# Optimization experiments

Measured on AMD Instinct MI355X. Metric: run time of the kernel, lower is better.

The kernel has to match this reference:

```python
import jax, jax.numpy as jnp
import numpy as np

K = 2048  # num_embeddings
D = 64    # embedding_dim


def setup_inputs() -> dict:
    key = jax.random.key(0)
    k1, k2 = jax.random.split(key)
    inputs = jax.random.normal(k1, (64, 32, 32, D), dtype=jnp.float32)
    # tf.random_uniform_initializer default: U[0, 1)
    embeddings = jax.random.uniform(k2, (K, D), dtype=jnp.float32)
    return {"inputs": inputs, "embeddings": embeddings}


def reference(inputs, embeddings):
    input_shape = inputs.shape
    flat_inputs = inputs.reshape(-1, D)  # [N, D]
    distances = (
        jnp.sum(flat_inputs ** 2, axis=1, keepdims=True)
        - 2.0 * jnp.matmul(flat_inputs, embeddings.T)
        + jnp.sum(embeddings ** 2, axis=1)
    )
    encoding_indices = jnp.argmin(distances, axis=1)  # [N]
    quantized = embeddings[encoding_indices].reshape(input_shape)
    # straight-through estimator
    quantized = inputs + jax.lax.stop_gradient(quantized - inputs)
    return quantized, encoding_indices, flat_inputs
```

## Files before the change

### kernel.cpp

```cpp
#include <hip/hip_runtime.h>
#include <cfloat>

#define N_TOTAL 65536
#define DIM     64
#define NEMB    2048

typedef __attribute__((ext_vector_type(8))) _Float16 half8;
typedef __attribute__((ext_vector_type(4))) float    floatx4;

__global__ void prep_kernel(const float* __restrict__ emb,
                            half8* __restrict__ ehp, float* __restrict__ en) {
    const int t = blockIdx.x * 256 + threadIdx.x;
    {
        const int l   = t & 63;
        const int ks  = (t >> 6) & 1;
        const int g   = t >> 7;
        const int col = g * 16 + (l & 15);
        const int kb  = ks * 32 + (l >> 4) * 8;
        const float* s = emb + col * DIM + kb;
        float4 v0 = *(const float4*)s, v1 = *(const float4*)(s + 4);
        half8 hv;
        hv[0] = (_Float16)v0.x; hv[1] = (_Float16)v0.y;
        hv[2] = (_Float16)v0.z; hv[3] = (_Float16)v0.w;
        hv[4] = (_Float16)v1.x; hv[5] = (_Float16)v1.y;
        hv[6] = (_Float16)v1.z; hv[7] = (_Float16)v1.w;
        ehp[t] = hv;
    }
    if (t < NEMB * 4) {
        const int row = t >> 2, seg = t & 3;
        const float* s = emb + row * DIM + seg * 16;
        float acc = 0.f;
#pragma unroll
        for (int i = 0; i < 4; ++i) {
            float4 v = ((const float4*)s)[i];
            acc = fmaf(v.x, v.x, acc); acc = fmaf(v.y, v.y, acc);
            acc = fmaf(v.z, v.z, acc); acc = fmaf(v.w, v.w, acc);
        }
        acc += __shfl_xor(acc, 1, 64);
        acc += __shfl_xor(acc, 2, 64);
        if (seg == 0) en[row] = acc;
    }
}

__global__ __launch_bounds__(256, 4) void vq_mfma_kernel(
        const float* __restrict__ x, const float* __restrict__ emb,
        const char* __restrict__ ehb, const float* __restrict__ eng,
        float* __restrict__ quant, float* __restrict__ idxf,
        float* __restrict__ flat) {

    __shared__ float EnS[NEMB];
    __shared__ uint4 Mrg[2][64];

    const int t    = threadIdx.x;
    const int wave = t >> 6, lane = t & 63;
    const int n = lane & 15, q = lane >> 4;
    const int h = wave & 1, p = wave >> 1;
    const int blk0 = blockIdx.x * 64;
    const int row0 = blk0 + p * 32;

    {
        const float4* s4 = (const float4*)(x + (size_t)blk0 * DIM);
        float4*       d4 = (float4*)(flat + (size_t)blk0 * DIM);
#pragma unroll
        for (int i = 0; i < 4; ++i) d4[i * 256 + t] = s4[i * 256 + t];
    }
    {
        const float4* s4 = (const float4*)eng;
        float4*       d4 = (float4*)EnS;
#pragma unroll
        for (int i = 0; i < 2; ++i) d4[i * 256 + t] = s4[i * 256 + t];
    }

    half8 ah[2][2], al[2][2];
#pragma unroll
    for (int tl = 0; tl < 2; ++tl)
#pragma unroll
        for (int ks = 0; ks < 2; ++ks) {
            const float* pp = x + (size_t)(row0 + tl * 16 + n) * DIM + ks * 32 + q * 8;
            float4 v0 = *(const float4*)pp, v1 = *(const float4*)(pp + 4);
            float xv[8] = {v0.x, v0.y, v0.z, v0.w, v1.x, v1.y, v1.z, v1.w};
#pragma unroll
            for (int j = 0; j < 8; ++j) {
                _Float16 hh = (_Float16)xv[j];
                ah[tl][ks][j] = hh;
                al[tl][ks][j] = (_Float16)(xv[j] - (float)hh);
            }
        }

    __syncthreads();

    unsigned best[8], sec[8];
#pragma unroll
    for (int r = 0; r < 8; ++r) { best[r] = 0u; sec[r] = 0u; }

    const char* ebase = ehb + (size_t)h * 131072 + (size_t)lane * 16;

    half8 bbuf[2][4];
    float enc[2][2];
#pragma unroll
    for (int i = 0; i < 4; ++i)
        bbuf[0][i] = *(const half8*)(ebase + i * 1024);
#pragma unroll
    for (int s = 0; s < 2; ++s)
        enc[0][s] = EnS[h * 1024 + s * 16 + n];

#pragma unroll 2
    for (int tile = 0; tile < 32; ++tile) {
        const int buf = tile & 1;
        if (tile < 31) {
            const char* src = ebase + (size_t)(tile + 1) * 4096;
#pragma unroll
            for (int i = 0; i < 4; ++i)
                bbuf[buf ^ 1][i] = *(const half8*)(src + i * 1024);
#pragma unroll
            for (int s = 0; s < 2; ++s)
                enc[buf ^ 1][s] = EnS[h * 1024 + (tile + 1) * 32 + s * 16 + n];
        }

#pragma unroll
        for (int sub = 0; sub < 2; ++sub) {
            const int L = tile * 2 + sub;
            const float enh = fmaf(-0.5f, enc[buf][sub], 128.0f);
            floatx4 a0 = {enh, enh, enh, enh};
            floatx4 a1 = a0;
            half8 bk0 = bbuf[buf][sub * 2 + 0];
            half8 bk1 = bbuf[buf][sub * 2 + 1];
            a0 = __builtin_amdgcn_mfma_f32_16x16x32_f16(ah[0][0], bk0, a0, 0, 0, 0);
            a1 = __builtin_amdgcn_mfma_f32_16x16x32_f16(ah[1][0], bk0, a1, 0, 0, 0);
            a0 = __builtin_amdgcn_mfma_f32_16x16x32_f16(al[0][0], bk0, a0, 0, 0, 0);
            a1 = __builtin_amdgcn_mfma_f32_16x16x32_f16(al[1][0], bk0, a1, 0, 0, 0);
            a0 = __builtin_amdgcn_mfma_f32_16x16x32_f16(ah[0][1], bk1, a0, 0, 0, 0);
            a1 = __builtin_amdgcn_mfma_f32_16x16x32_f16(ah[1][1], bk1, a1, 0, 0, 0);
            a0 = __builtin_amdgcn_mfma_f32_16x16x32_f16(al[0][1], bk1, a0, 0, 0, 0);
            a1 = __builtin_amdgcn_mfma_f32_16x16x32_f16(al[1][1], bk1, a1, 0, 0, 0);

            const unsigned Lp = (unsigned)(63 - L);
#pragma unroll
            for (int r = 0; r < 8; ++r) {
                float v = (r < 4) ? a0[r] : a1[r - 4];
                unsigned key = (__float_as_uint(v) & 0xFFFFFFC0u) | Lp;
                unsigned lo  = best[r] < key ? best[r] : key;
                best[r] = best[r] > key ? best[r] : key;
                sec[r]  = sec[r] > lo ? sec[r] : lo;
            }
        }
    }

    unsigned bval[8], bcol[8], sval[8], scol[8];
#pragma unroll
    for (int r = 0; r < 8; ++r) {
        bval[r] = best[r] & 0xFFFFFFC0u;
        bcol[r] = (unsigned)(h * 1024 + (63 - (int)(best[r] & 63u)) * 16 + n);
        sval[r] = sec[r] & 0xFFFFFFC0u;
        scol[r] = (unsigned)(h * 1024 + (63 - (int)(sec[r] & 63u)) * 16 + n);
    }
#pragma unroll
    for (int m = 1; m < 16; m <<= 1) {
#pragma unroll
        for (int r = 0; r < 8; ++r) {
            unsigned ov  = (unsigned)__shfl_xor((int)bval[r], m, 64);
            unsigned oc  = (unsigned)__shfl_xor((int)bcol[r], m, 64);
            unsigned ov2 = (unsigned)__shfl_xor((int)sval[r], m, 64);
            unsigned oc2 = (unsigned)__shfl_xor((int)scol[r], m, 64);
            bool ow = (ov > bval[r]) || (ov == bval[r] && oc < bcol[r]);
            unsigned nbv = ow ? ov : bval[r], nbc = ow ? oc : bcol[r];
            unsigned lv  = ow ? bval[r] : ov, lc  = ow ? bcol[r] : oc;
            bool sv2 = (ov2 > sval[r]) || (ov2 == sval[r] && oc2 < scol[r]);
            unsigned bsv = sv2 ? ov2 : sval[r], bsc = sv2 ? oc2 : scol[r];
            bool s3 = (lv > bsv) || (lv == bsv && lc < bsc);
            sval[r] = s3 ? lv : bsv; scol[r] = s3 ? lc : bsc;
            bval[r] = nbv; bcol[r] = nbc;
        }
    }
    if (n == 0) {
#pragma unroll
        for (int r = 0; r < 8; ++r) {
            const int lr = p * 32 + (r >> 2) * 16 + q * 4 + (r & 3);
            Mrg[h][lr] = make_uint4(bval[r], bcol[r], sval[r], scol[r]);
        }
    }
    __syncthreads();

#pragma unroll
    for (int r = 0; r < 4; ++r) {
        const int lr   = wave * 16 + q * 4 + r;
        const int grow = blk0 + lr;
        uint4 c0v = Mrg[0][lr], c1v = Mrg[1][lr];
        int cand[4] = {(int)c0v.y, (int)c0v.w, (int)c1v.y, (int)c1v.w};
        float4 xv = *(const float4*)(x + (size_t)grow * DIM + n * 4);
        float pbest = -FLT_MAX; int cbest = 0;
        float4 ebest = {0.f, 0.f, 0.f, 0.f};
#pragma unroll
        for (int c = 0; c < 4; ++c) {
            float4 e = *(const float4*)(emb + (size_t)cand[c] * DIM + n * 4);
            float pp = (xv.x - 0.5f * e.x) * e.x + (xv.y - 0.5f * e.y) * e.y
                     + (xv.z - 0.5f * e.z) * e.z + (xv.w - 0.5f * e.w) * e.w;
#pragma unroll
            for (int m2 = 1; m2 < 16; m2 <<= 1) pp += __shfl_xor(pp, m2, 64);
            bool take = (pp > pbest) || (pp == pbest && cand[c] < cbest);
            pbest = take ? pp : pbest;
            cbest = take ? cand[c] : cbest;
            ebest.x = take ? e.x : ebest.x; ebest.y = take ? e.y : ebest.y;
            ebest.z = take ? e.z : ebest.z; ebest.w = take ? e.w : ebest.w;
        }
        *(float4*)(quant + (size_t)grow * DIM + n * 4) = ebest;
        if (n == 0) idxf[grow] = (float)cbest;
    }
}

extern "C" void kernel_launch(void* const* d_in, const int* in_sizes, int n_in,
                              void* d_out, int out_size, void* d_ws, size_t ws_size,
                              hipStream_t stream) {
    const float* x   = (const float*)d_in[0];
    const float* emb = (const float*)d_in[1];
    float* out   = (float*)d_out;
    float* quant = out;
    float* idxf  = out + (size_t)N_TOTAL * DIM;
    float* flat  = idxf + N_TOTAL;

    half8* ehp = (half8*)d_ws;
    float* en  = (float*)((char*)d_ws + (size_t)NEMB * DIM * 2);

    prep_kernel<<<64, 256, 0, stream>>>(emb, ehp, en);
    vq_mfma_kernel<<<N_TOTAL / 64, 256, 0, stream>>>(x, emb, (const char*)ehp, en,
                                                     quant, idxf, flat);
}
```

Measured before the change: 122.2 us.

## Read codebook norms from global, use med3 top-2 update and MFMA priority

Drops the LDS staging of codebook norms and the barrier before the main loop, so each lane reads its norm values straight from global memory. Replaces the min/max second-best update with a single v_med3_u32 and keeps the key mask in a VGPR via inline asm. Raises wave priority around the MFMA chain with s_setprio and shares one broadcast accumulator init between both tiles. The aim is fewer ALU instructions per candidate and no startup barrier, at the cost of global-memory norm loads inside the loop.

```diff
diff --git a/kernel.cpp b/kernel.cpp
--- a/kernel.cpp
+++ b/kernel.cpp
@@ -48,7 +48,6 @@
         float* __restrict__ quant, float* __restrict__ idxf,
         float* __restrict__ flat) {
 
-    __shared__ float EnS[NEMB];
     __shared__ uint4 Mrg[2][64];
 
     const int t    = threadIdx.x;
@@ -64,12 +63,6 @@
 #pragma unroll
         for (int i = 0; i < 4; ++i) d4[i * 256 + t] = s4[i * 256 + t];
     }
-    {
-        const float4* s4 = (const float4*)eng;
-        float4*       d4 = (float4*)EnS;
-#pragma unroll
-        for (int i = 0; i < 2; ++i) d4[i * 256 + t] = s4[i * 256 + t];
-    }
 
     half8 ah[2][2], al[2][2];
 #pragma unroll
@@ -87,22 +80,23 @@
             }
         }
 
-    __syncthreads();
+    unsigned maskv;
+    asm("v_mov_b32 %0, 0xFFFFFFC0" : "=v"(maskv));
 
     unsigned best[8], sec[8];
 #pragma unroll
     for (int r = 0; r < 8; ++r) { best[r] = 0u; sec[r] = 0u; }
 
-    const char* ebase = ehb + (size_t)h * 131072 + (size_t)lane * 16;
+    const char*  ebase = ehb + (size_t)h * 131072 + (size_t)lane * 16;
+    const float* enp   = eng + h * 1024 + n;
 
     half8 bbuf[2][4];
     float enc[2][2];
 #pragma unroll
     for (int i = 0; i < 4; ++i)
         bbuf[0][i] = *(const half8*)(ebase + i * 1024);
-#pragma unroll
-    for (int s = 0; s < 2; ++s)
-        enc[0][s] = EnS[h * 1024 + s * 16 + n];
+    enc[0][0] = enp[0];
+    enc[0][1] = enp[16];
 
 #pragma unroll 2
     for (int tile = 0; tile < 32; ++tile) {
@@ -112,36 +106,39 @@
 #pragma unroll
             for (int i = 0; i < 4; ++i)
                 bbuf[buf ^ 1][i] = *(const half8*)(src + i * 1024);
-#pragma unroll
-            for (int s = 0; s < 2; ++s)
-                enc[buf ^ 1][s] = EnS[h * 1024 + (tile + 1) * 32 + s * 16 + n];
+            enc[buf ^ 1][0] = enp[(tile + 1) * 32];
+            enc[buf ^ 1][1] = enp[(tile + 1) * 32 + 16];
         }
 
 #pragma unroll
         for (int sub = 0; sub < 2; ++sub) {
             const int L = tile * 2 + sub;
             const float enh = fmaf(-0.5f, enc[buf][sub], 128.0f);
-            floatx4 a0 = {enh, enh, enh, enh};
-            floatx4 a1 = a0;
+            floatx4 e4 = {enh, enh, enh, enh};
             half8 bk0 = bbuf[buf][sub * 2 + 0];
             half8 bk1 = bbuf[buf][sub * 2 + 1];
-            a0 = __builtin_amdgcn_mfma_f32_16x16x32_f16(ah[0][0], bk0, a0, 0, 0, 0);
-            a1 = __builtin_amdgcn_mfma_f32_16x16x32_f16(ah[1][0], bk0, a1, 0, 0, 0);
+            __builtin_amdgcn_s_setprio(1);
+            floatx4 a0 = __builtin_amdgcn_mfma_f32_16x16x32_f16(ah[0][0], bk0, e4, 0, 0, 0);
+            floatx4 a1 = __builtin_amdgcn_mfma_f32_16x16x32_f16(ah[1][0], bk0, e4, 0, 0, 0);
             a0 = __builtin_amdgcn_mfma_f32_16x16x32_f16(al[0][0], bk0, a0, 0, 0, 0);
             a1 = __builtin_amdgcn_mfma_f32_16x16x32_f16(al[1][0], bk0, a1, 0, 0, 0);
             a0 = __builtin_amdgcn_mfma_f32_16x16x32_f16(ah[0][1], bk1, a0, 0, 0, 0);
             a1 = __builtin_amdgcn_mfma_f32_16x16x32_f16(ah[1][1], bk1, a1, 0, 0, 0);
             a0 = __builtin_amdgcn_mfma_f32_16x16x32_f16(al[0][1], bk1, a0, 0, 0, 0);
             a1 = __builtin_amdgcn_mfma_f32_16x16x32_f16(al[1][1], bk1, a1, 0, 0, 0);
+            __builtin_amdgcn_s_setprio(0);
 
             const unsigned Lp = (unsigned)(63 - L);
 #pragma unroll
             for (int r = 0; r < 8; ++r) {
                 float v = (r < 4) ? a0[r] : a1[r - 4];
-                unsigned key = (__float_as_uint(v) & 0xFFFFFFC0u) | Lp;
-                unsigned lo  = best[r] < key ? best[r] : key;
-                best[r] = best[r] > key ? best[r] : key;
-                sec[r]  = sec[r] > lo ? sec[r] : lo;
+                unsigned key = (__float_as_uint(v) & maskv) | Lp;
+                unsigned nb  = best[r] > key ? best[r] : key;
+                unsigned ns;
+                asm("v_med3_u32 %0, %1, %2, %3"
+                    : "=v"(ns) : "v"(best[r]), "v"(sec[r]), "v"(key));
+                sec[r]  = ns;
+                best[r] = nb;
             }
         }
     }
```

After: 120.0 us. No clear change (-1.8%).
